# Kernel optimization log

Measured on AMD Instinct MI355X. Metric: run time of the kernel, lower is better.

Reference implementation:

```python
import jax, jax.numpy as jnp
import numpy as np

D_MODEL = 768
H = 6
DQK = 128
DV = 256
SCALE_BASE = 512.0


def _xpos(x, sign):
    """xPos rotary: x (B,T,H,d); sign=+1 for queries, -1 for keys."""
    B, T, Hn, d = x.shape
    half = d // 2
    pos = jnp.arange(T, dtype=jnp.float32)
    inv_freq = 1.0 / (10000.0 ** (jnp.arange(half, dtype=jnp.float32) / half))
    angles = pos[:, None] * inv_freq[None, :]                    # (T, half)
    zeta = (jnp.arange(half, dtype=jnp.float32) + half) / d      # (half,)
    decay = zeta[None, :] ** (sign * pos[:, None] / SCALE_BASE)  # (T, half)
    cos_a = (jnp.cos(angles) * decay)[None, :, None, :]
    sin_a = (jnp.sin(angles) * decay)[None, :, None, :]
    x1, x2 = x[..., :half], x[..., half:]
    return jnp.concatenate([x1 * cos_a - x2 * sin_a,
                            x1 * sin_a + x2 * cos_a], axis=-1)


def _decay_mask(T):
    """(H,T,T) causal decay mask, row-normalized by sqrt(row_sum)."""
    gammas = jnp.array([1.0 - 2.0 ** (-(5 + h)) for h in range(H)], dtype=jnp.float32)
    i = jnp.arange(T, dtype=jnp.float32)
    diff = i[:, None] - i[None, :]
    causal = (diff >= 0).astype(jnp.float32)
    D = (gammas[:, None, None] ** jnp.clip(diff, 0.0)[None]) * causal[None]
    row = jnp.clip(jnp.sum(D, axis=-1, keepdims=True), 1e-6)
    return D / jnp.sqrt(row)


def setup_inputs() -> dict:
    key = jax.random.key(0)
    ks = jax.random.split(key, 6)
    B, T = 2, 2048

    def xavier(k, shape):
        lim = float(np.sqrt(6.0 / (shape[0] + shape[1])))
        return jax.random.uniform(k, shape, jnp.float32, -lim, lim)

    return {
        "x": jax.random.normal(ks[0], (B, T, D_MODEL), jnp.float32),
        "Wq": xavier(ks[1], (D_MODEL, H * DQK)),
        "Wk": xavier(ks[2], (D_MODEL, H * DQK)),
        "Wv": xavier(ks[3], (D_MODEL, H * DV)),
        "Wg": xavier(ks[4], (D_MODEL, H * DV)),
        "Wo": xavier(ks[5], (H * DV, D_MODEL)),
        "gn_weight": jnp.ones((H * DV,), jnp.float32),
        "gn_bias": jnp.zeros((H * DV,), jnp.float32),
    }


def reference(x, Wq, Wk, Wv, Wg, Wo, gn_weight, gn_bias):
    B, T, _ = x.shape
    Q = (x @ Wq).reshape(B, T, H, DQK)
    K = (x @ Wk).reshape(B, T, H, DQK)
    V = (x @ Wv).reshape(B, T, H, DV)
    Q = _xpos(Q, 1.0)
    K = _xpos(K, -1.0)
    # retention scores: QK^T * scale * per-head decay mask (no softmax)
    scores = jnp.einsum('bihd,bjhd->bhij', Q, K) * (DQK ** -0.5)
    scores = scores * _decay_mask(T)[None]
    out = jnp.einsum('bhij,bjhv->bihv', scores, V)   # (B,T,H,DV)
    concat = out.reshape(B, T, H * DV)
    # GroupNorm over (channels-in-group, time) per (batch, group), as torch GN on (B,C,T)
    g = concat.transpose(0, 2, 1).reshape(B, H, DV, T)
    mean = jnp.mean(g, axis=(2, 3), keepdims=True)
    var = jnp.var(g, axis=(2, 3), keepdims=True)
    g = (g - mean) / jnp.sqrt(var + 1e-5)
    g = g.reshape(B, H * DV, T) * gn_weight[None, :, None] + gn_bias[None, :, None]
    normed = g.transpose(0, 2, 1)                    # (B,T,H*DV)
    gate = jax.nn.silu(x @ Wg)
    return (normed * gate) @ Wo
```

## Files before the change

kernel.cpp:

```cpp
#include <hip/hip_runtime.h>

typedef unsigned short u16;
typedef unsigned int u32;
typedef __attribute__((ext_vector_type(8))) short short8;
typedef __attribute__((ext_vector_type(4))) float f32x4;

#define DEV static __device__ __forceinline__

DEV float bf2f(u16 u){ u32 i = ((u32)u)<<16; float f; __builtin_memcpy(&f,&i,4); return f; }
DEV u16 f2bf(float f){ u32 i; __builtin_memcpy(&i,&f,4); u32 r = i + 0x7FFFu + ((i>>16)&1u); return (u16)(r>>16); }

DEV void gld16(const void* gp, void* lp){
  __builtin_amdgcn_global_load_lds((const __attribute__((address_space(1))) void*)gp,
                                   (__attribute__((address_space(3))) void*)lp, 16, 0, 0);
}

__global__ void k_prep(const float* __restrict__ x,
                       const float* __restrict__ Wq, const float* __restrict__ Wk,
                       const float* __restrict__ Wv, const float* __restrict__ Wg,
                       const float* __restrict__ Wo,
                       u16* __restrict__ xb, u16* __restrict__ WT, u16* __restrict__ WoT,
                       float4* __restrict__ tab){
  __shared__ float tile[32][33];
  int i = blockIdx.x, tid = threadIdx.x;
  if (i < 3072){
    size_t base = ((size_t)i*256 + tid)*4;
    float4 v = *(const float4*)(x + base);
    ushort4 o; o.x=f2bf(v.x); o.y=f2bf(v.y); o.z=f2bf(v.z); o.w=f2bf(v.w);
    *(ushort4*)(xb + base) = o;
  } else if (i < 7680){
    int j = i - 3072;
    const float* src; u16* dst; int N, K, bx, by;
    if (j < 576)       { src=Wq; dst=WT;             N=768;  K=768;  bx=j%24; by=j/24; }
    else if (j < 1152) { int q=j-576;  src=Wk; dst=WT+768ull*768;  N=768;  K=768;  bx=q%24; by=q/24; }
    else if (j < 2304) { int q=j-1152; src=Wv; dst=WT+1536ull*768; N=1536; K=768;  bx=q%48; by=q/48; }
    else if (j < 3456) { int q=j-2304; src=Wg; dst=WT+3072ull*768; N=1536; K=768;  bx=q%48; by=q/48; }
    else               { int q=j-3456; src=Wo; dst=WoT;            N=768;  K=1536; bx=q%24; by=q/24; }
    int n0 = bx*32, k0 = by*32;
    int tx = tid&31, ty = tid>>5;
    #pragma unroll
    for (int q=0;q<4;++q)
      tile[ty + q*8][tx] = src[(size_t)(k0 + ty + q*8)*N + n0 + tx];
    __syncthreads();
    #pragma unroll
    for (int q=0;q<4;++q)
      dst[(size_t)(n0 + ty + q*8)*K + k0 + tx] = f2bf(tile[tx][ty + q*8]);
  } else {
    int idx = (i-7680)*256 + tid;
    int t = idx>>6, j = idx&63;
    float inv_freq = expf(-(float)j * (9.210340371976184f/64.f));
    float angle = (float)t * inv_freq;
    float zeta = (float)(j + 64) * (1.f/128.f);
    float decq = exp2f(log2f(zeta) * ((float)t*(1.f/512.f)));
    float deck = 1.f/decq;
    float sn, cs; sincosf(angle, &sn, &cs);
    float4 o; o.x = cs*decq; o.y = sn*decq; o.z = cs*deck; o.w = sn*deck;
    tab[idx] = o;
  }
}

__global__ void k_xpos2(u16* __restrict__ Qr, u16* __restrict__ Kr, const float4* __restrict__ tab){
  int idx = blockIdx.x*256 + threadIdx.x;
  int jg = idx & 15;
  int h  = (idx>>4) % 6;
  int m  = (idx>>4) / 6;
  int t  = m & 2047;
  size_t base = (size_t)m*768 + h*128 + jg*4;
  ushort4 q1 = *(const ushort4*)(Qr + base);
  ushort4 q2 = *(const ushort4*)(Qr + base + 64);
  ushort4 k1 = *(const ushort4*)(Kr + base);
  ushort4 k2 = *(const ushort4*)(Kr + base + 64);
  ushort4 oq1, oq2, ok1, ok2;
  const float4* tb = tab + t*64 + jg*4;
  #pragma unroll
  for (int jj=0;jj<4;++jj){
    float4 f = tb[jj];
    float a, b2;
    a = bf2f(((const u16*)&q1)[jj]); b2 = bf2f(((const u16*)&q2)[jj]);
    ((u16*)&oq1)[jj] = f2bf(a*f.x - b2*f.y);
    ((u16*)&oq2)[jj] = f2bf(a*f.y + b2*f.x);
    a = bf2f(((const u16*)&k1)[jj]); b2 = bf2f(((const u16*)&k2)[jj]);
    ((u16*)&ok1)[jj] = f2bf(a*f.z - b2*f.w);
    ((u16*)&ok2)[jj] = f2bf(a*f.w + b2*f.z);
  }
  *(ushort4*)(Qr + base)      = oq1;
  *(ushort4*)(Qr + base + 64) = oq2;
  *(ushort4*)(Kr + base)      = ok1;
  *(ushort4*)(Kr + base + 64) = ok2;
}

__global__ void k_trans(const u16* __restrict__ Vraw, u16* __restrict__ VbTs,
                        const u16* __restrict__ Kr, u16* __restrict__ KbT){
  __shared__ u16 tile[32][33];
  int i = blockIdx.x, tid = threadIdx.x;
  int tx = tid&31, ty = tid>>5;
  if (i < 6144){
    int bh = i>>9, r = i&511;
    int t0 = (r&63)*32, v0 = (r>>6)*32;
    int b = bh/6, h = bh%6;
    float lg2g = log2f(1.f - exp2f(-(float)(5+h)));
    float dec = exp2f(lg2g * (float)(63 - ((t0 + tx) & 63)));
    #pragma unroll
    for (int q=0;q<4;++q)
      tile[ty+q*8][tx] = Vraw[(size_t)(b*2048 + t0 + ty + q*8)*1536 + h*256 + v0 + tx];
    __syncthreads();
    #pragma unroll
    for (int q=0;q<4;++q)
      VbTs[(size_t)(bh*256 + v0 + ty + q*8)*2048 + t0 + tx] = f2bf(bf2f(tile[tx][ty+q*8]) * dec);
  } else {
    int j = i - 6144;
    int bh = j>>8, r = j&255;
    int t0 = (r&63)*32, d0 = (r>>6)*32;
    int b = bh/6, h = bh%6;
    #pragma unroll
    for (int q=0;q<4;++q)
      tile[ty+q*8][tx] = Kr[(size_t)(b*2048 + t0 + ty + q*8)*768 + h*128 + d0 + tx];
    __syncthreads();
    #pragma unroll
    for (int q=0;q<4;++q)
      KbT[(size_t)(bh*128 + d0 + ty + q*8)*2048 + t0 + tx] = tile[tx][ty+q*8];
  }
}

template<int MODE, int BM>
__global__ __launch_bounds__(256)
void k_gemm(const u16* __restrict__ A, const u16* __restrict__ BT,
            int K, int N,
            u16* __restrict__ Qr, u16* __restrict__ Kr,
            u16* __restrict__ Vraw, u16* __restrict__ Gb,
            float* __restrict__ Out)
{
  constexpr int MR = BM/32;
  __shared__ u16 As[BM*64];
  __shared__ u16 Bs[128*64];
  const int tid = threadIdx.x;
  const int w = tid>>6, l = tid&63, g = l>>4, ln = l&15;
  const int wr = w>>1, wc = w&1;
  const int m0 = blockIdx.x*BM, n0 = blockIdx.y*128;
  const f32x4 fz = {0.f,0.f,0.f,0.f};
  f32x4 acc[MR][4];
  #pragma unroll
  for (int m=0;m<MR;++m)
    #pragma unroll
    for (int n=0;n<4;++n) acc[m][n] = fz;

  const int nk = K>>6;
  for (int kt=0; kt<nk; ++kt){
    const int k0 = kt<<6;
    #pragma unroll
    for (int i=0;i<BM/32;++i){
      int off = i*4096 + tid*16;
      int row = off>>7;
      int colb = (off&127) ^ ((row&7)<<4);
      gld16(A  + (size_t)(m0+row)*K + k0 + (colb>>1), (char*)As + i*4096 + w*1024);
    }
    #pragma unroll
    for (int i=0;i<4;++i){
      int off = i*4096 + tid*16;
      int row = off>>7;
      int colb = (off&127) ^ ((row&7)<<4);
      gld16(BT + (size_t)(n0+row)*K + k0 + (colb>>1), (char*)Bs + i*4096 + w*1024);
    }
    __syncthreads();
    #pragma unroll
    for (int kk=0;kk<2;++kk){
      short8 a[MR], b[4];
      #pragma unroll
      for (int m=0;m<MR;++m){
        int row = wr*(BM/2) + m*16 + ln;
        int byte = row*128 + ((kk*64 + g*16) ^ ((row&7)<<4));
        a[m] = *(const short8*)((const char*)As + byte);
      }
      #pragma unroll
      for (int n=0;n<4;++n){
        int row = wc*64 + n*16 + ln;
        int byte = row*128 + ((kk*64 + g*16) ^ ((row&7)<<4));
        b[n] = *(const short8*)((const char*)Bs + byte);
      }
      #pragma unroll
      for (int m=0;m<MR;++m)
        #pragma unroll
        for (int n=0;n<4;++n)
          acc[m][n] = __builtin_amdgcn_mfma_f32_16x16x32_bf16(a[m], b[n], acc[m][n], 0,0,0);
    }
    __syncthreads();
  }
  const int region = n0/768;
  #pragma unroll
  for (int m=0;m<MR;++m){
    int grow0 = m0 + wr*(BM/2) + m*16 + g*4;
    #pragma unroll
    for (int n=0;n<4;++n){
      int c = n0 + wc*64 + n*16 + ln;
      #pragma unroll
      for (int r=0;r<4;++r){
        float v = acc[m][n][r];
        size_t grow = (size_t)(grow0 + r);
        if (MODE == 1){
          Out[grow*(size_t)N + c] = v;
        } else {
          if (region==0)      Qr[grow*768 + c] = f2bf(v);
          else if (region==1) Kr[grow*768 + (c-768)] = f2bf(v);
          else if (region<4)  Vraw[grow*1536 + (c-1536)] = f2bf(v);
          else { float sg = v/(1.f+__expf(-v)); Gb[grow*1536 + (c-3072)] = f2bf(sg); }
        }
      }
    }
  }
}

__global__ __launch_bounds__(256)
void k_passA(const u16* __restrict__ VbTs, const u16* __restrict__ KbT, u16* __restrict__ Zb)
{
  __shared__ u16 Kt[128*64];
  __shared__ u16 Vt[256*64];
  const int tid = threadIdx.x, w = tid>>6, l = tid&63, g = l>>4, ln = l&15;
  const int c = blockIdx.x, bh = blockIdx.y;
  const f32x4 fz = {0.f,0.f,0.f,0.f};

  #pragma unroll
  for (int i=0;i<4;++i){
    int off = i*4096 + tid*16;
    int row = off>>7;
    int colb = (off&127) ^ ((row&7)<<4);
    gld16(KbT + (size_t)(bh*128 + row)*2048 + c*64 + (colb>>1), (char*)Kt + i*4096 + w*1024);
  }
  #pragma unroll
  for (int i=0;i<8;++i){
    int off = i*4096 + tid*16;
    int row = off>>7;
    int colb = (off&127) ^ ((row&7)<<4);
    gld16(VbTs + (size_t)(bh*256 + row)*2048 + c*64 + (colb>>1), (char*)Vt + i*4096 + w*1024);
  }
  __syncthreads();

  f32x4 acc[4][8];
  #pragma unroll
  for (int m=0;m<4;++m)
    #pragma unroll
    for (int n=0;n<8;++n) acc[m][n] = fz;

  #pragma unroll
  for (int kk=0;kk<2;++kk){
    short8 va[4], kb[8];
    #pragma unroll
    for (int m=0;m<4;++m){
      int vrow = w*64 + m*16 + ln;
      int byte = vrow*128 + ((kk*64 + g*16) ^ ((vrow&7)<<4));
      va[m] = *(const short8*)((const char*)Vt + byte);
    }
    #pragma unroll
    for (int n=0;n<8;++n){
      int krow = n*16 + ln;
      int byte = krow*128 + ((kk*64 + g*16) ^ ((krow&7)<<4));
      kb[n] = *(const short8*)((const char*)Kt + byte);
    }
    #pragma unroll
    for (int m=0;m<4;++m)
      #pragma unroll
      for (int n=0;n<8;++n)
        acc[m][n] = __builtin_amdgcn_mfma_f32_16x16x32_bf16(va[m], kb[n], acc[m][n], 0,0,0);
  }

  u16* z = Zb + (size_t)(c*12 + bh)*32768;
  #pragma unroll
  for (int m=0;m<4;++m)
    #pragma unroll
    for (int n=0;n<8;++n)
      #pragma unroll
      for (int r=0;r<4;++r){
        int v = w*64 + m*16 + g*4 + r;
        int d = n*16 + ln;
        z[v*128 + d] = f2bf(acc[m][n][r]);
      }
}

__global__ __launch_bounds__(256)
void k_scan(const u16* __restrict__ Zb, u16* __restrict__ States)
{
  int gid = blockIdx.x*256 + threadIdx.x;
  int bh = gid >> 13;
  int e0 = (gid & 8191) * 4;
  const int h = bh % 6;
  const float lg2g = log2f(1.f - exp2f(-(float)(5+h)));
  const float gl = exp2f(lg2g * 64.f);
  ushort4 z[31];
  #pragma unroll
  for (int c=0;c<31;++c)
    z[c] = *(const ushort4*)(Zb + (size_t)(c*12 + bh)*32768 + e0);
  {
    ushort4 o; o.x=0;o.y=0;o.z=0;o.w=0;
    *(ushort4*)(States + (size_t)bh*32768 + e0) = o;
  }
  float S0=0.f,S1=0.f,S2=0.f,S3=0.f;
  #pragma unroll
  for (int c=1;c<32;++c){
    ushort4 zz = z[c-1];
    S0 = gl*S0 + bf2f(zz.x); S1 = gl*S1 + bf2f(zz.y);
    S2 = gl*S2 + bf2f(zz.z); S3 = gl*S3 + bf2f(zz.w);
    ushort4 o; o.x=f2bf(S0); o.y=f2bf(S1); o.z=f2bf(S2); o.w=f2bf(S3);
    *(ushort4*)(States + (size_t)(c*12 + bh)*32768 + e0) = o;
  }
}

__global__ __launch_bounds__(256)
void k_passC(const u16* __restrict__ Qb, const u16* __restrict__ Kb,
             const u16* __restrict__ VbTs, const u16* __restrict__ States,
             u16* __restrict__ Ofb, float* __restrict__ partials)
{
  __shared__ u16 Ks[64*128];
  __shared__ u16 Vt[256*64];
  __shared__ float Ps[64*64];
  __shared__ float red[8];
  const int tid = threadIdx.x, w = tid>>6, l = tid&63, g = l>>4, ln = l&15;
  const int c = blockIdx.x, bh = blockIdx.y, b = bh/6, h = bh%6;
  const float omg = exp2f(-(float)(5+h));
  const float gamma = 1.f - omg;
  const float lg2g = log2f(gamma);
  const float scale = 0.08838834764831845f;
  const int q0 = c*64;
  const f32x4 fz = {0.f,0.f,0.f,0.f};

  short8 aq[4];
  {
    const size_t qrow = (size_t)(b*2048 + q0 + w*16 + ln)*768 + h*128;
    #pragma unroll
    for (int kk=0;kk<4;++kk) aq[kk] = *(const short8*)(Qb + qrow + kk*32 + g*8);
  }

  #pragma unroll
  for (int i=0;i<4;++i){
    int off = i*4096 + tid*16;
    int row = off>>8;
    int colb = (off&255) ^ ((row&7)<<4);
    gld16(Kb + (size_t)(b*2048 + q0 + row)*768 + h*128 + (colb>>1),
          (char*)Ks + i*4096 + w*1024);
  }
  #pragma unroll
  for (int i=0;i<8;++i){
    int off = i*4096 + tid*16;
    int row = off>>7;
    int colb = (off&127) ^ ((row&7)<<4);
    gld16(VbTs + (size_t)(bh*256 + row)*2048 + q0 + (colb>>1),
          (char*)Vt + i*4096 + w*1024);
  }
  __syncthreads();

  f32x4 sacc[4]; sacc[0]=fz; sacc[1]=fz; sacc[2]=fz; sacc[3]=fz;
  #pragma unroll
  for (int kk=0;kk<4;++kk){
    #pragma unroll
    for (int n=0;n<4;++n){
      int row = n*16 + ln;
      int byte = row*256 + ((kk*64 + g*16) ^ ((row&7)<<4));
      short8 bk = *(const short8*)((const char*)Ks + byte);
      sacc[n] = __builtin_amdgcn_mfma_f32_16x16x32_bf16(aq[kk], bk, sacc[n], 0,0,0);
    }
  }
  #pragma unroll
  for (int n=0;n<4;++n){
    int kj = n*16 + ln;
    #pragma unroll
    for (int r=0;r<4;++r){
      int a = w*16 + g*4 + r;
      float p = (a >= kj) ? sacc[n][r] : 0.f;
      int prow = w*16 + g*4 + r;
      int byte = prow*256 + ((((n*16+ln)*4)) ^ ((prow&7)<<4));
      *(float*)((char*)Ps + byte) = p;
    }
  }
  f32x4 acc[16];
  #pragma unroll
  for (int i=0;i<16;++i) acc[i] = fz;
  #pragma unroll
  for (int kk2=0;kk2<2;++kk2){
    int prow = w*16 + ln;
    int base = prow*256;
    int c0 = kk2*128 + g*32;
    int sw = (prow&7)<<4;
    f32x4 p0 = *(const f32x4*)((const char*)Ps + base + ((c0   )^sw));
    f32x4 p1 = *(const f32x4*)((const char*)Ps + base + ((c0+16)^sw));
    short8 ap;
    #pragma unroll
    for (int jj=0;jj<4;++jj){ ap[jj] = (short)f2bf(p0[jj]); ap[4+jj] = (short)f2bf(p1[jj]); }
    #pragma unroll
    for (int n2=0;n2<16;++n2){
      int vrow = n2*16 + ln;
      int byte = vrow*128 + ((kk2*64 + g*16) ^ ((vrow&7)<<4));
      short8 bv = *(const short8*)((const char*)Vt + byte);
      acc[n2] = __builtin_amdgcn_mfma_f32_16x16x32_bf16(ap, bv, acc[n2], 0,0,0);
    }
  }
  const float gi64 = exp2f(-64.f*lg2g);
  #pragma unroll
  for (int i=0;i<16;++i){ acc[i][0]*=gi64; acc[i][1]*=gi64; acc[i][2]*=gi64; acc[i][3]*=gi64; }
  const u16* st = States + (size_t)(c*12 + bh)*32768;
  #pragma unroll
  for (int kk=0;kk<4;++kk){
    #pragma unroll
    for (int n2=0;n2<16;++n2){
      short8 sb = *(const short8*)(st + (n2*16 + ln)*128 + kk*32 + g*8);
      acc[n2] = __builtin_amdgcn_mfma_f32_16x16x32_bf16(aq[kk], sb, acc[n2], 0,0,0);
    }
  }
  float rf[4];
  #pragma unroll
  for (int r=0;r<4;++r){
    int a = w*16 + g*4 + r;
    int qi = q0 + a;
    float rs = (1.f - exp2f(lg2g*(float)(qi+1))) / omg;
    rf[r] = scale * exp2f(lg2g*(float)(a+1)) * rsqrtf(fmaxf(rs, 1e-6f));
  }
  float lsum=0.f, lsq=0.f;
  #pragma unroll
  for (int n2=0;n2<16;++n2){
    #pragma unroll
    for (int r=0;r<4;++r){
      float v = acc[n2][r]*rf[r];
      Ofb[(size_t)(b*2048 + q0 + w*16 + g*4 + r)*1536 + h*256 + n2*16 + ln] = f2bf(v);
      lsum += v; lsq += v*v;
    }
  }
  #pragma unroll
  for (int o=32;o;o>>=1){ lsum += __shfl_xor(lsum,o,64); lsq += __shfl_xor(lsq,o,64); }
  if (l==0){ red[w*2]=lsum; red[w*2+1]=lsq; }
  __syncthreads();
  if (tid==0){
    partials[(c*12+bh)*2]   = red[0]+red[2]+red[4]+red[6];
    partials[(c*12+bh)*2+1] = red[1]+red[3]+red[5]+red[7];
  }
}

__global__ __launch_bounds__(256)
void k_gatenorm(const u16* __restrict__ Ofb, const u16* __restrict__ Gb,
                const float* __restrict__ gnw, const float* __restrict__ gnb,
                const float* __restrict__ partials, u16* __restrict__ Yb){
  const int bh = blockIdx.y, b = bh/6, h = bh%6;
  const int tid = threadIdx.x, l = tid&63;
  float s=0.f, q=0.f;
  if (l < 32){ s = partials[(l*12+bh)*2]; q = partials[(l*12+bh)*2+1]; }
  #pragma unroll
  for (int o=16;o;o>>=1){ s += __shfl_xor(s,o,64); q += __shfl_xor(q,o,64); }
  s = __shfl(s, 0, 64); q = __shfl(q, 0, 64);
  const float Ninv = 1.f/524288.f;
  float mean = s*Ninv;
  float var = q*Ninv - mean*mean;
  float rstd = rsqrtf(var + 1e-5f);

  int t = blockIdx.x*8 + (tid>>5);
  int v0 = (tid&31)*8;
  size_t base = (size_t)(b*2048 + t)*1536 + h*256 + v0;
  int cidx = h*256 + v0;
  short8 ov = *(const short8*)(Ofb + base);
  short8 gv = *(const short8*)(Gb + base);
  short8 yo;
  #pragma unroll
  for (int jj=0;jj<8;++jj){
    float o = bf2f((u16)ov[jj]);
    float nv = (o-mean)*rstd*gnw[cidx+jj] + gnb[cidx+jj];
    yo[jj] = (short)f2bf(nv * bf2f((u16)gv[jj]));
  }
  *(short8*)(Yb + base) = yo;
}

extern "C" void kernel_launch(void* const* d_in, const int* in_sizes, int n_in,
                              void* d_out, int out_size, void* d_ws, size_t ws_size,
                              hipStream_t stream)
{
  const float* x   = (const float*)d_in[0];
  const float* Wq  = (const float*)d_in[1];
  const float* Wk  = (const float*)d_in[2];
  const float* Wv  = (const float*)d_in[3];
  const float* Wg  = (const float*)d_in[4];
  const float* Wo  = (const float*)d_in[5];
  const float* gnw = (const float*)d_in[6];
  const float* gnb = (const float*)d_in[7];
  float* out = (float*)d_out;

  char* ws = (char*)d_ws;
  u16*   xb     = (u16*)  (ws + 0);
  u16*   WT     = (u16*)  (ws + 6291456);
  u16*   Vraw   = (u16*)  (ws + 13369344);
  u16*   KbT    = (u16*)  (ws + 6291456);
  u16*   States = (u16*)  (ws + 0);
  u16*   Yb     = (u16*)  (ws + 0);
  u16*   Kr     = (u16*)  (ws + 25952256);
  u16*   Qr     = (u16*)  (ws + 32243712);
  u16*   Gb     = (u16*)  (ws + 38535168);
  u16*   WoT    = (u16*)  (ws + 51118080);
  u16*   VbTs   = (u16*)  (ws + 53477376);
  u16*   Zb     = (u16*)  (ws + 66060288);
  u16*   Ofb    = (u16*)  (ws + 66060288);
  float* partials = (float*)(ws + 91226112);
  float4* tab   = (float4*)(ws + 95158272);

  k_prep<<<8192, 256, 0, stream>>>(x, Wq, Wk, Wv, Wg, Wo, xb, WT, WoT, tab);
  k_gemm<0,128><<<dim3(32,36), 256, 0, stream>>>(xb, WT, 768, 4608, Qr, Kr, Vraw, Gb, (float*)nullptr);
  k_xpos2<<<1536, 256, 0, stream>>>(Qr, Kr, tab);
  k_trans<<<9216, 256, 0, stream>>>(Vraw, VbTs, Kr, KbT);
  k_passA<<<dim3(31,12), 256, 0, stream>>>(VbTs, KbT, Zb);
  k_scan<<<384, 256, 0, stream>>>(Zb, States);
  k_passC<<<dim3(32,12), 256, 0, stream>>>(Qr, Kr, VbTs, States, Ofb, partials);
  k_gatenorm<<<dim3(256,12), 256, 0, stream>>>(Ofb, Gb, gnw, gnb, partials, Yb);
  k_gemm<1,64><<<dim3(64,6), 256, 0, stream>>>(Yb, WoT, 1536, 768,
                                            (u16*)nullptr,(u16*)nullptr,(u16*)nullptr,(u16*)nullptr,
                                            out);
}
```

Baseline: 150.5 us.

## Replace QKVG projection GEMM with 256x256-tile, 8-wave, double-buffered LDS kernel

The fused Q/K/V/G projection GEMM moves from a 128x128 tile with 256 threads to a new 256x256 tile with 512 threads (8 waves, 128x64 per wave). It double-buffers 128KB of LDS filled by direct global-to-LDS loads, uses an XOR swizzle to avoid bank conflicts, splits each K-step into half-steps so loads overlap MFMA, and raises wave priority around the MFMA bursts. The goal is more data reuse per byte loaded and better overlap of memory with compute. The cost is only 288 blocks at one block per CU because of the LDS footprint, so occupancy is low and wave-quantization effects are possible.

```diff
diff --git a/kernel.cpp b/kernel.cpp
--- a/kernel.cpp
+++ b/kernel.cpp
@@ -13,6 +13,12 @@
 DEV void gld16(const void* gp, void* lp){
   __builtin_amdgcn_global_load_lds((const __attribute__((address_space(1))) void*)gp,
                                    (__attribute__((address_space(3))) void*)lp, 16, 0, 0);
+}
+
+DEV void bar(){
+  asm volatile("" ::: "memory");
+  __builtin_amdgcn_s_barrier();
+  asm volatile("" ::: "memory");
 }
 
 __global__ void k_prep(const float* __restrict__ x,
@@ -122,6 +128,139 @@
   }
 }
 
+__global__ __launch_bounds__(512)
+void k_gemm0(const u16* __restrict__ A, const u16* __restrict__ BT,
+             u16* __restrict__ Qr, u16* __restrict__ Kr,
+             u16* __restrict__ Vraw, u16* __restrict__ Gb)
+{
+  constexpr int K = 768;
+  __shared__ u16 lds[65536];
+  char* sm = (char*)lds;
+  const int tid = threadIdx.x;
+  const int w = tid>>6, l = tid&63, g = l>>4, ln = l&15;
+  const int wm = w>>2, wn = w&3;
+  const int m0 = blockIdx.x*256, n0 = blockIdx.y*256;
+  const f32x4 fz = {0.f,0.f,0.f,0.f};
+  f32x4 acc[8][4];
+  #pragma unroll
+  for (int m=0;m<8;++m)
+    #pragma unroll
+    for (int n=0;n<4;++n) acc[m][n] = fz;
+
+  auto stA = [&](int buf, int kt, int kh){
+    #pragma unroll
+    for (int i=0;i<2;++i){
+      int off = i*8192 + tid*16;
+      int row = off>>6;
+      int s = off&63;
+      int kcol = (s ^ ((((row)>>1)&3)<<4)) >> 1;
+      gld16(A + (size_t)(m0+row)*K + kt*64 + kh*32 + kcol,
+            sm + buf*32768 + kh*16384 + i*8192 + w*1024);
+    }
+  };
+  auto stB = [&](int buf, int kt, int kh){
+    #pragma unroll
+    for (int i=0;i<2;++i){
+      int off = i*8192 + tid*16;
+      int row = off>>6;
+      int s = off&63;
+      int kcol = (s ^ ((((row)>>1)&3)<<4)) >> 1;
+      gld16(BT + (size_t)(n0+row)*K + kt*64 + kh*32 + kcol,
+            sm + 65536 + buf*32768 + kh*16384 + i*8192 + w*1024);
+    }
+  };
+
+  short8 a[8], b0[2], b1[2];
+  auto lda = [&](int buf, int kk){
+    #pragma unroll
+    for (int m=0;m<8;++m){
+      int row = wm*128 + m*16 + ln;
+      a[m] = *(const short8*)(sm + buf*32768 + kk*16384 + row*64 + ((g*16) ^ ((((row)>>1)&3)<<4)));
+    }
+  };
+  auto ldb = [&](short8* b, int buf, int kk, int nq){
+    #pragma unroll
+    for (int ni=0;ni<2;++ni){
+      int row = wn*64 + (nq*2+ni)*16 + ln;
+      b[ni] = *(const short8*)(sm + 65536 + buf*32768 + kk*16384 + row*64 + ((g*16) ^ ((((row)>>1)&3)<<4)));
+    }
+  };
+
+  stA(0,0,0); stB(0,0,0); stA(0,0,1); stB(0,0,1);
+
+  const int nt = K/64;
+  for (int j=0; j<nt; ++j){
+    const int cur = j&1, nxt = cur^1;
+    const bool hn = (j+1 < nt);
+    asm volatile("s_waitcnt vmcnt(4)" ::: "memory");
+    __builtin_amdgcn_sched_barrier(0);
+    bar();
+    lda(cur, 0);
+    ldb(b0, cur, 0, 0);
+    if (hn) stA(nxt, j+1, 0);
+    __builtin_amdgcn_s_setprio(1);
+    #pragma unroll
+    for (int m=0;m<8;++m){
+      acc[m][0] = __builtin_amdgcn_mfma_f32_16x16x32_bf16(a[m], b0[0], acc[m][0], 0,0,0);
+      acc[m][1] = __builtin_amdgcn_mfma_f32_16x16x32_bf16(a[m], b0[1], acc[m][1], 0,0,0);
+    }
+    __builtin_amdgcn_s_setprio(0);
+    bar();
+    ldb(b1, cur, 0, 1);
+    if (hn) stB(nxt, j+1, 0);
+    __builtin_amdgcn_s_setprio(1);
+    #pragma unroll
+    for (int m=0;m<8;++m){
+      acc[m][2] = __builtin_amdgcn_mfma_f32_16x16x32_bf16(a[m], b1[0], acc[m][2], 0,0,0);
+      acc[m][3] = __builtin_amdgcn_mfma_f32_16x16x32_bf16(a[m], b1[1], acc[m][3], 0,0,0);
+    }
+    __builtin_amdgcn_s_setprio(0);
+    if (hn) asm volatile("s_waitcnt vmcnt(4)" ::: "memory");
+    else    asm volatile("s_waitcnt vmcnt(0)" ::: "memory");
+    __builtin_amdgcn_sched_barrier(0);
+    bar();
+    lda(cur, 1);
+    ldb(b0, cur, 1, 0);
+    if (hn) stA(nxt, j+1, 1);
+    __builtin_amdgcn_s_setprio(1);
+    #pragma unroll
+    for (int m=0;m<8;++m){
+      acc[m][0] = __builtin_amdgcn_mfma_f32_16x16x32_bf16(a[m], b0[0], acc[m][0], 0,0,0);
+      acc[m][1] = __builtin_amdgcn_mfma_f32_16x16x32_bf16(a[m], b0[1], acc[m][1], 0,0,0);
+    }
+    __builtin_amdgcn_s_setprio(0);
+    bar();
+    ldb(b1, cur, 1, 1);
+    if (hn) stB(nxt, j+1, 1);
+    __builtin_amdgcn_s_setprio(1);
+    #pragma unroll
+    for (int m=0;m<8;++m){
+      acc[m][2] = __builtin_amdgcn_mfma_f32_16x16x32_bf16(a[m], b1[0], acc[m][2], 0,0,0);
+      acc[m][3] = __builtin_amdgcn_mfma_f32_16x16x32_bf16(a[m], b1[1], acc[m][3], 0,0,0);
+    }
+    __builtin_amdgcn_s_setprio(0);
+  }
+
+  const int region = n0/768;
+  #pragma unroll
+  for (int m=0;m<8;++m){
+    int grow0 = m0 + wm*128 + m*16 + g*4;
+    #pragma unroll
+    for (int n=0;n<4;++n){
+      int c = n0 + wn*64 + n*16 + ln;
+      #pragma unroll
+      for (int r=0;r<4;++r){
+        float v = acc[m][n][r];
+        size_t grow = (size_t)(grow0 + r);
+        if (region==0)      Qr[grow*768 + c] = f2bf(v);
+        else if (region==1) Kr[grow*768 + (c-768)] = f2bf(v);
+        else if (region<4)  Vraw[grow*1536 + (c-1536)] = f2bf(v);
+        else { float sg = v/(1.f+__expf(-v)); Gb[grow*1536 + (c-3072)] = f2bf(sg); }
+      }
+    }
+  }
+}
+
 template<int MODE, int BM>
 __global__ __launch_bounds__(256)
 void k_gemm(const u16* __restrict__ A, const u16* __restrict__ BT,
@@ -495,7 +634,7 @@
   float4* tab   = (float4*)(ws + 95158272);
 
   k_prep<<<8192, 256, 0, stream>>>(x, Wq, Wk, Wv, Wg, Wo, xb, WT, WoT, tab);
-  k_gemm<0,128><<<dim3(32,36), 256, 0, stream>>>(xb, WT, 768, 4608, Qr, Kr, Vraw, Gb, (float*)nullptr);
+  k_gemm0<<<dim3(16,18), 512, 0, stream>>>(xb, WT, Qr, Kr, Vraw, Gb);
   k_xpos2<<<1536, 256, 0, stream>>>(Qr, Kr, tab);
   k_trans<<<9216, 256, 0, stream>>>(Vraw, VbTs, Kr, KbT);
   k_passA<<<dim3(31,12), 256, 0, stream>>>(VbTs, KbT, Zb);
```

Measured after the change: 173.5 us. 15.3% more time.
